# Kernel tuning notes

Measured on AMD Instinct MI355X. Metric: run time of the kernel, lower is better.

Reference implementation:

```python
import jax, jax.numpy as jnp
import numpy as np

C = 384
NUM_HEADS = 12
WS = 12  # window side
N = WS * WS  # tokens per window = 144
NW = 144  # windows per image
BATCH = 8

def setup_inputs() -> dict:
    key = jax.random.key(0)
    k1, k2, k3, k4, k5, k6, k7 = jax.random.split(key, 7)
    x = jax.random.normal(k1, (BATCH, NW, WS, WS, C), dtype=jnp.float32)
    mask = jax.random.normal(k2, (NW, N, N), dtype=jnp.float32)
    s = 1.0 / np.sqrt(C)
    qkv_w = jax.random.normal(k3, (3 * C, C), dtype=jnp.float32) * s
    qkv_b = jax.random.normal(k4, (3 * C,), dtype=jnp.float32) * 0.02
    proj_w = jax.random.normal(k5, (C, C), dtype=jnp.float32) * s
    proj_b = jax.random.normal(k6, (C,), dtype=jnp.float32) * 0.02
    return {"x": x, "mask": mask, "qkv_w": qkv_w, "qkv_b": qkv_b,
            "proj_w": proj_w, "proj_b": proj_b}

def reference(x, mask, qkv_w, qkv_b, proj_w, proj_b):
    B, nW = x.shape[0], x.shape[1]
    head_dim = C // NUM_HEADS
    scale = head_dim ** -0.5
    # (B_, N, C) windowed tokens
    xw = x.reshape(B * nW, N, C)
    qkv = jnp.einsum('bnc,dc->bnd', xw, qkv_w) + qkv_b  # (B_, N, 3C)
    qkv = qkv.reshape(B * nW, N, 3, NUM_HEADS, head_dim)
    q = qkv[:, :, 0].transpose(0, 2, 1, 3) * scale  # (B_, H, N, hd)
    k = qkv[:, :, 1].transpose(0, 2, 1, 3)
    v = qkv[:, :, 2].transpose(0, 2, 1, 3)
    attn = jnp.einsum('bhnd,bhmd->bhnm', q, k)  # (B_, H, N, N)
    # add window mask: view as (B, nW, H, N, N) + mask[None, :, None]
    attn = attn.reshape(B, nW, NUM_HEADS, N, N) + mask[None, :, None, :, :]
    attn = jax.nn.softmax(attn.reshape(B * nW, NUM_HEADS, N, N), axis=-1)
    out = jnp.einsum('bhnm,bhmd->bhnd', attn, v)  # (B_, H, N, hd)
    out = out.transpose(0, 2, 1, 3).reshape(B * nW, N, C)
    out = jnp.einsum('bnc,dc->bnd', out, proj_w) + proj_b
    return out
```

## Files before the change

### kernel.cpp

```cpp
#include <hip/hip_runtime.h>
#include <stdint.h>

#define TOK 144
#define CD  384
#define NH  12
#define HDIM 32
#define NWIN 1152
#define MASKW 144
#define NQKV 1152

typedef __bf16 bf16_t;
typedef __bf16 bf16x4 __attribute__((ext_vector_type(4)));
typedef __bf16 bf16x8 __attribute__((ext_vector_type(8)));
typedef float  f32x4  __attribute__((ext_vector_type(4)));

__device__ __forceinline__ void gload16(const void* g, void* l) {
    __builtin_amdgcn_global_load_lds(
        (const __attribute__((address_space(1))) uint32_t*)g,
        (__attribute__((address_space(3))) uint32_t*)l, 16, 0, 0);
}

__global__ __launch_bounds__(256) void kpack(const float* __restrict__ qkvw,
                                             const float* __restrict__ projw,
                                             bf16_t* __restrict__ WQf,
                                             bf16_t* __restrict__ WPf)
{
    int t = blockIdx.x * 256 + threadIdx.x;
    const int NQU = 55296;
    const float SCALE = 0.17677669529663687f;
    if (t < NQU) {
        int lane = t & 63;
        int jj = (t >> 6) & 7;
        int kh = (t >> 9) & 1;
        int rest = t >> 10;
        int kk = rest % 6, nb = rest / 6;
        int d = nb * 128 + jj * 16 + (lane & 15);
        int k = kk * 64 + kh * 32 + (lane >> 4) * 8;
        const float* src = qkvw + (size_t)d * 384 + k;
        float4 a = *(const float4*)src;
        float4 b = *(const float4*)(src + 4);
        float s = (d < 384) ? SCALE : 1.0f;
        bf16x8 o = {(bf16_t)(a.x*s), (bf16_t)(a.y*s), (bf16_t)(a.z*s), (bf16_t)(a.w*s),
                    (bf16_t)(b.x*s), (bf16_t)(b.y*s), (bf16_t)(b.z*s), (bf16_t)(b.w*s)};
        *(bf16x8*)(WQf + (size_t)t * 8) = o;
    } else {
        int u = t - NQU;
        int lane = u & 63;
        int jj = (u >> 6) & 7;
        int kh = (u >> 9) & 1;
        int rest = u >> 10;
        int kk = rest % 6, nb = rest / 6;
        int d = nb * 128 + jj * 16 + (lane & 15);
        int k = kk * 64 + kh * 32 + (lane >> 4) * 8;
        const float* src = projw + (size_t)d * 384 + k;
        float4 a = *(const float4*)src;
        float4 b = *(const float4*)(src + 4);
        bf16x8 o = {(bf16_t)a.x, (bf16_t)a.y, (bf16_t)a.z, (bf16_t)a.w,
                    (bf16_t)b.x, (bf16_t)b.y, (bf16_t)b.z, (bf16_t)b.w};
        *(bf16x8*)(WPf + (size_t)u * 8) = o;
    }
}

__global__ __launch_bounds__(256) void kmask(const float* __restrict__ mask,
                                             float* __restrict__ maskR)
{
    int t = blockIdx.x * 256 + threadIdx.x;
    int lane = t & 63;
    int g = t >> 6;
    int nt = g % 9;
    int g2 = g / 9;
    int wv = g2 % 9;
    int wm = g2 / 9;
    const float* src = mask + (size_t)wm * 20736
                     + (wv * 16 + (lane >> 4) * 4) * 144 + nt * 16 + (lane & 15);
    f32x4 v = { src[0], src[144], src[288], src[432] };
    *(f32x4*)(maskR + (size_t)t * 4) = v;
}

__global__ __launch_bounds__(256) void kx(const float* __restrict__ x,
                                          bf16_t* __restrict__ xb, int n8)
{
    int i = blockIdx.x * 256 + threadIdx.x;
    if (i < n8) {
        float4 a = *(const float4*)(x + (size_t)i * 8);
        float4 b = *(const float4*)(x + (size_t)i * 8 + 4);
        bf16x8 o = {(bf16_t)a.x, (bf16_t)a.y, (bf16_t)a.z, (bf16_t)a.w,
                    (bf16_t)b.x, (bf16_t)b.y, (bf16_t)b.z, (bf16_t)b.w};
        *(bf16x8*)(xb + (size_t)i * 8) = o;
    }
}

__global__ __launch_bounds__(256) void k_qkv(const bf16_t* __restrict__ xb,
                                             const bf16_t* __restrict__ WQf,
                                             const float* __restrict__ bias,
                                             bf16_t* __restrict__ Qp,
                                             bf16_t* __restrict__ Kp,
                                             bf16_t* __restrict__ VTp)
{
    int nwg = gridDim.x;
    int orig = blockIdx.x;
    int q8 = nwg >> 3, r8 = nwg & 7;
    int xcd = orig & 7, idx = orig >> 3;
    int wgid = (xcd < r8 ? xcd * (q8 + 1) : r8 * (q8 + 1) + (xcd - r8) * q8) + idx;
    int mb = wgid / 9, nb = wgid % 9;

    __shared__ union SMem {
        bf16_t A[2][128 * 64];
        bf16_t tile[128 * 136];
    } sm;

    int tid = threadIdx.x;
    int lane = tid & 63, wid = tid >> 6;
    int wr = (wid >> 1) * 64, wc = (wid & 1) * 64;
    int l15 = lane & 15, l4 = lane >> 4;
    int lr8 = lane >> 3, lc8 = lane & 7;
    int lc8s = lc8 ^ lr8;

    f32x4 acc[4][4] = {};

    const bf16_t* aG = xb + ((size_t)mb * 128 + wid * 32 + lr8) * 384 + lc8s * 8;

    #pragma unroll
    for (int p = 0; p < 4; ++p)
        gload16(aG + (size_t)p * (8 * 384), &sm.A[0][(wid * 4 + p) * 512]);

    for (int kk = 0; kk < 6; ++kk) {
        int buf = kk & 1;
        __syncthreads();
        if (kk < 5) {
            #pragma unroll
            for (int p = 0; p < 4; ++p)
                gload16(aG + (size_t)p * (8 * 384) + (kk + 1) * 64,
                        &sm.A[buf ^ 1][(wid * 4 + p) * 512]);
        }
        #pragma unroll
        for (int kh = 0; kh < 2; ++kh) {
            bf16x8 af[4], bfr[4];
            #pragma unroll
            for (int j = 0; j < 4; ++j)
                bfr[j] = *(const bf16x8*)(WQf +
                    ((((size_t)(nb * 6 + kk) * 2 + kh) * 8 + (wid & 1) * 4 + j) * 64 + lane) * 8);
            #pragma unroll
            for (int i = 0; i < 4; ++i) {
                int row = wr + i * 16 + l15;
                int slot = (kh * 4 + l4) ^ (l15 & 7);
                af[i] = *(const bf16x8*)&sm.A[buf][row * 64 + slot * 8];
            }
            #pragma unroll
            for (int i = 0; i < 4; ++i)
                #pragma unroll
                for (int j = 0; j < 4; ++j)
                    acc[i][j] = __builtin_amdgcn_mfma_f32_16x16x32_bf16(af[i], bfr[j], acc[i][j], 0, 0, 0);
        }
    }
    __syncthreads();

    const int S = 136;
    const float SCALE = 0.17677669529663687f;
    float scl = (nb < 3) ? SCALE : 1.0f;
    float bv[4];
    #pragma unroll
    for (int j = 0; j < 4; ++j) bv[j] = bias[nb * 128 + wc + j * 16 + l15] * scl;

    #pragma unroll
    for (int i = 0; i < 4; ++i)
        #pragma unroll
        for (int j = 0; j < 4; ++j)
            #pragma unroll
            for (int r = 0; r < 4; ++r)
                sm.tile[(wr + i * 16 + l4 * 4 + r) * S + wc + j * 16 + l15] =
                    (bf16_t)(acc[i][j][r] + bv[j]);
    __syncthreads();

    if (nb < 6) {
        bf16_t* dst = (nb < 3) ? Qp : Kp;
        int db0 = (nb % 3) * 128;
        #pragma unroll
        for (int it = 0; it < 8; ++it) {
            int item = tid + it * 256;
            int row = item >> 4, ch = item & 15;
            bf16x8 v = *(const bf16x8*)&sm.tile[row * S + ch * 8];
            int gr = mb * 128 + row;
            int lw = gr / 144, n = gr - lw * 144;
            int dl = db0 + ch * 8;
            int h = dl >> 5, c32 = dl & 31;
            *(bf16x8*)(dst + (size_t)(lw * 12 + h) * 4608 + n * 32 + c32) = v;
        }
    } else {
        int db0 = (nb - 6) * 128;
        #pragma unroll
        for (int it = 0; it < 8; ++it) {
            int item = tid + it * 256;
            int dl = item & 127;
            int nc = item >> 7;
            int gr0 = mb * 128 + nc * 8;
            int lw = gr0 / 144, n0 = gr0 - lw * 144;
            int rr = db0 + dl;
            int h = rr >> 5, j32 = rr & 31;
            bf16x8 v;
            #pragma unroll
            for (int q = 0; q < 8; ++q)
                v[q] = sm.tile[(nc * 8 + q) * S + dl];
            *(bf16x8*)(VTp + (size_t)(lw * 12 + h) * 4608 + j32 * 144 + n0) = v;
        }
    }
}

__global__ __launch_bounds__(576) void k_attn(const bf16_t* __restrict__ Qp,
                                              const bf16_t* __restrict__ Kp,
                                              const bf16_t* __restrict__ VTp,
                                              const float* __restrict__ maskR,
                                              bf16_t* __restrict__ ao,
                                              int w0)
{
    extern __shared__ char smem[];
    bf16_t* kb  = (bf16_t*)smem;
    bf16_t* vtb = kb + 144 * 40;
    bf16_t* pb  = vtb + 32 * 168;

    int nwg = gridDim.x;
    int orig = blockIdx.x;
    int q8 = nwg >> 3, r8 = nwg & 7;
    int xcd = orig & 7, idx = orig >> 3;
    int wgid = (xcd < r8 ? xcd * (q8 + 1) : r8 * (q8 + 1) + (xcd - r8) * q8) + idx;

    int bw = wgid / 12, h = wgid % 12;
    int W = w0 + bw;
    int wm = W % MASKW;
    size_t base = (size_t)(bw * 12 + h) * 4608;
    int tid = threadIdx.x;

    {
        int row = tid >> 2, c8 = (tid & 3) * 8;
        *(uint4*)&kb[row * 40 + c8] = *(const uint4*)(Kp + base + row * 32 + c8);
        int j = tid / 18, seg = tid % 18;
        *(uint4*)&vtb[j * 168 + seg * 8] = *(const uint4*)(VTp + base + j * 144 + seg * 8);
        if (tid < 64) {
            int jj = tid >> 1, cc = 144 + (tid & 1) * 8;
            uint4 z = {0, 0, 0, 0};
            *(uint4*)&vtb[jj * 168 + cc] = z;
        }
    }
    __syncthreads();

    int lane = tid & 63, wv = tid >> 6;
    int l15 = lane & 15, l4 = lane >> 4;
    int row16 = wv * 16;

    bf16x8 aq = *(const bf16x8*)(Qp + base + (row16 + l15) * 32 + l4 * 8);

    const float* mR = maskR + ((size_t)(wm * 9 + wv) * 9) * 256 + lane * 4;
    f32x4 s[9];
    #pragma unroll
    for (int nt = 0; nt < 9; ++nt) {
        bf16x8 bk = *(const bf16x8*)&kb[(nt * 16 + l15) * 40 + l4 * 8];
        f32x4 mv = *(const f32x4*)(mR + nt * 256);
        s[nt] = __builtin_amdgcn_mfma_f32_16x16x32_bf16(aq, bk, mv, 0, 0, 0);
    }

    float mx[4], sm[4];
    #pragma unroll
    for (int r = 0; r < 4; ++r) {
        float m = s[0][r];
        #pragma unroll
        for (int nt = 1; nt < 9; ++nt) m = fmaxf(m, s[nt][r]);
        #pragma unroll
        for (int off = 1; off < 16; off <<= 1) m = fmaxf(m, __shfl_xor(m, off, 64));
        mx[r] = m;
    }
    #pragma unroll
    for (int r = 0; r < 4; ++r) {
        float sum = 0.f;
        #pragma unroll
        for (int nt = 0; nt < 9; ++nt) {
            float e = __expf(s[nt][r] - mx[r]);
            s[nt][r] = e;
            sum += e;
        }
        #pragma unroll
        for (int off = 1; off < 16; off <<= 1) sum += __shfl_xor(sum, off, 64);
        sm[r] = sum;
    }

    #pragma unroll
    for (int nt = 0; nt < 9; ++nt)
        #pragma unroll
        for (int r = 0; r < 4; ++r)
            pb[(row16 + l4 * 4 + r) * 168 + nt * 16 + l15] = (bf16_t)s[nt][r];
    {
        int rr = lane >> 2, cc = 144 + (lane & 3) * 4;
        uint2 z = {0, 0};
        *(uint2*)&pb[(row16 + rr) * 168 + cc] = z;
    }
    f32x4 o0 = {0.f, 0.f, 0.f, 0.f}, o1 = {0.f, 0.f, 0.f, 0.f};
    #pragma unroll
    for (int ks = 0; ks < 5; ++ks) {
        bf16x8 ap  = *(const bf16x8*)&pb[(row16 + l15) * 168 + ks * 32 + l4 * 8];
        bf16x8 bv0 = *(const bf16x8*)&vtb[(l15) * 168 + ks * 32 + l4 * 8];
        bf16x8 bv1 = *(const bf16x8*)&vtb[(16 + l15) * 168 + ks * 32 + l4 * 8];
        o0 = __builtin_amdgcn_mfma_f32_16x16x32_bf16(ap, bv0, o0, 0, 0, 0);
        o1 = __builtin_amdgcn_mfma_f32_16x16x32_bf16(ap, bv1, o1, 0, 0, 0);
    }
    float inv[4];
    #pragma unroll
    for (int r = 0; r < 4; ++r) inv[r] = 1.0f / sm[r];
    bf16_t* ob = pb + row16 * 168;
    #pragma unroll
    for (int r = 0; r < 4; ++r) {
        ob[(l4 * 4 + r) * 32 + l15]      = (bf16_t)(o0[r] * inv[r]);
        ob[(l4 * 4 + r) * 32 + 16 + l15] = (bf16_t)(o1[r] * inv[r]);
    }
    bf16x8 v = *(const bf16x8*)&ob[(lane >> 2) * 32 + (lane & 3) * 8];
    *(bf16x8*)(ao + ((size_t)bw * 144 + row16 + (lane >> 2)) * 384 + h * 32 + (lane & 3) * 8) = v;
}

__global__ __launch_bounds__(256) void k_proj(const bf16_t* __restrict__ ao,
                                              const bf16_t* __restrict__ WPf,
                                              const float* __restrict__ bias,
                                              float* __restrict__ out,
                                              int rowoff)
{
    int nwg = gridDim.x;
    int orig = blockIdx.x;
    int q8 = nwg >> 3, r8 = nwg & 7;
    int xcd = orig & 7, idx = orig >> 3;
    int wgid = (xcd < r8 ? xcd * (q8 + 1) : r8 * (q8 + 1) + (xcd - r8) * q8) + idx;
    int mb = wgid / 3, nb = wgid % 3;

    __shared__ union SMem {
        bf16_t A[2][128 * 64];
        float tile[128 * 68];
    } sm;

    int tid = threadIdx.x;
    int lane = tid & 63, wid = tid >> 6;
    int wr = (wid >> 1) * 64, wc = (wid & 1) * 64;
    int l15 = lane & 15, l4 = lane >> 4;
    int lr8 = lane >> 3, lc8 = lane & 7;
    int lc8s = lc8 ^ lr8;

    f32x4 acc[4][4] = {};

    const bf16_t* aG = ao + ((size_t)mb * 128 + wid * 32 + lr8) * 384 + lc8s * 8;

    #pragma unroll
    for (int p = 0; p < 4; ++p)
        gload16(aG + (size_t)p * (8 * 384), &sm.A[0][(wid * 4 + p) * 512]);

    for (int kk = 0; kk < 6; ++kk) {
        int buf = kk & 1;
        __syncthreads();
        if (kk < 5) {
            #pragma unroll
            for (int p = 0; p < 4; ++p)
                gload16(aG + (size_t)p * (8 * 384) + (kk + 1) * 64,
                        &sm.A[buf ^ 1][(wid * 4 + p) * 512]);
        }
        #pragma unroll
        for (int kh = 0; kh < 2; ++kh) {
            bf16x8 af[4], bfr[4];
            #pragma unroll
            for (int j = 0; j < 4; ++j)
                bfr[j] = *(const bf16x8*)(WPf +
                    ((((size_t)(nb * 6 + kk) * 2 + kh) * 8 + (wid & 1) * 4 + j) * 64 + lane) * 8);
            #pragma unroll
            for (int i = 0; i < 4; ++i) {
                int row = wr + i * 16 + l15;
                int slot = (kh * 4 + l4) ^ (l15 & 7);
                af[i] = *(const bf16x8*)&sm.A[buf][row * 64 + slot * 8];
            }
            #pragma unroll
            for (int i = 0; i < 4; ++i)
                #pragma unroll
                for (int j = 0; j < 4; ++j)
                    acc[i][j] = __builtin_amdgcn_mfma_f32_16x16x32_bf16(af[i], bfr[j], acc[i][j], 0, 0, 0);
        }
    }
    __syncthreads();

    float bv[4];
    #pragma unroll
    for (int j = 0; j < 4; ++j) bv[j] = bias[nb * 128 + wc + j * 16 + l15];

    #pragma unroll
    for (int half = 0; half < 2; ++half) {
        if (half) __syncthreads();
        if ((wid & 1) == half) {
            #pragma unroll
            for (int i = 0; i < 4; ++i)
                #pragma unroll
                for (int j = 0; j < 4; ++j)
                    #pragma unroll
                    for (int r = 0; r < 4; ++r)
                        sm.tile[(wr + i * 16 + l4 * 4 + r) * 68 + j * 16 + l15] =
                            acc[i][j][r] + bv[j];
        }
        __syncthreads();
        #pragma unroll
        for (int it = 0; it < 8; ++it) {
            int item = tid + it * 256;
            int row = item >> 4, ch = item & 15;
            float4 v = *(const float4*)&sm.tile[row * 68 + ch * 4];
            *(float4*)(out + (size_t)(rowoff + mb * 128 + row) * 384
                           + nb * 128 + half * 64 + ch * 4) = v;
        }
    }
}

extern "C" void kernel_launch(void* const* d_in, const int* in_sizes, int n_in,
                              void* d_out, int out_size, void* d_ws, size_t ws_size,
                              hipStream_t stream)
{
    const float* x     = (const float*)d_in[0];
    const float* mask  = (const float*)d_in[1];
    const float* qkvw  = (const float*)d_in[2];
    const float* qkvb  = (const float*)d_in[3];
    const float* projw = (const float*)d_in[4];
    const float* projb = (const float*)d_in[5];
    float* out = (float*)d_out;

    char* ws = (char*)d_ws;
    bf16_t* WQf  = (bf16_t*)ws;
    bf16_t* WPf  = (bf16_t*)(ws + 884736);
    float* maskR = (float*)(ws + 1179648);
    char* chunkbase = ws + 13123584;

    size_t avail = ws_size > 13123584 ? ws_size - 13123584 : 0;
    long cw = (long)(avail / 552960);
    cw = (cw / 16) * 16;
    if (cw > NWIN) cw = NWIN;
    if (cw < 16) cw = 16;

    size_t qbytes = (size_t)cw * 110592;
    bf16_t* Xb  = (bf16_t*)chunkbase;
    bf16_t* Qp  = (bf16_t*)(chunkbase + qbytes);
    bf16_t* Kp  = (bf16_t*)(chunkbase + 2 * qbytes);
    bf16_t* VTp = (bf16_t*)(chunkbase + 3 * qbytes);
    bf16_t* AO  = (bf16_t*)(chunkbase + 4 * qbytes);

    kpack<<<288, 256, 0, stream>>>(qkvw, projw, WQf, WPf);
    kmask<<<2916, 256, 0, stream>>>(mask, maskR);

    for (int w0 = 0; w0 < NWIN; w0 += (int)cw) {
        int c = (int)((NWIN - w0) < cw ? (NWIN - w0) : cw);
        int n8 = c * 6912;
        kx<<<(n8 + 255) / 256, 256, 0, stream>>>(x + (size_t)w0 * 144 * 384, Xb, n8);
        int mblocks = (c * 144) / 128;
        k_qkv<<<mblocks * 9, 256, 0, stream>>>(Xb, WQf, qkvb, Qp, Kp, VTp);
        k_attn<<<c * 12, 576, 70656, stream>>>(Qp, Kp, VTp, maskR, AO, w0);
        k_proj<<<mblocks * 3, 256, 0, stream>>>(AO, WPf, projb, out, w0 * 144);
    }
}
```

Baseline: 647.6 us.

## Load GEMM A fragments directly from global instead of LDS double buffering

Both the QKV and projection GEMM kernels drop their async global-to-LDS double-buffered staging of the A tile. Each wave now reads its MFMA A fragments straight from global memory, relying on L1/L2 for reuse across the two waves that share rows. This removes the per-k-step barriers and the LDS traffic, and shrinks shared memory to just the epilogue tile, which may raise occupancy. The cost is redundant global loads and exposed load latency without explicit prefetch.

```diff
diff --git a/kernel.cpp b/kernel.cpp
--- a/kernel.cpp
+++ b/kernel.cpp
@@ -13,12 +13,6 @@
 typedef __bf16 bf16x4 __attribute__((ext_vector_type(4)));
 typedef __bf16 bf16x8 __attribute__((ext_vector_type(8)));
 typedef float  f32x4  __attribute__((ext_vector_type(4)));
-
-__device__ __forceinline__ void gload16(const void* g, void* l) {
-    __builtin_amdgcn_global_load_lds(
-        (const __attribute__((address_space(1))) uint32_t*)g,
-        (__attribute__((address_space(3))) uint32_t*)l, 16, 0, 0);
-}
 
 __global__ __launch_bounds__(256) void kpack(const float* __restrict__ qkvw,
                                              const float* __restrict__ projw,
@@ -104,48 +98,28 @@
     int wgid = (xcd < r8 ? xcd * (q8 + 1) : r8 * (q8 + 1) + (xcd - r8) * q8) + idx;
     int mb = wgid / 9, nb = wgid % 9;
 
-    __shared__ union SMem {
-        bf16_t A[2][128 * 64];
-        bf16_t tile[128 * 136];
-    } sm;
+    __shared__ bf16_t tile[128 * 136];
 
     int tid = threadIdx.x;
     int lane = tid & 63, wid = tid >> 6;
     int wr = (wid >> 1) * 64, wc = (wid & 1) * 64;
     int l15 = lane & 15, l4 = lane >> 4;
-    int lr8 = lane >> 3, lc8 = lane & 7;
-    int lc8s = lc8 ^ lr8;
 
     f32x4 acc[4][4] = {};
 
-    const bf16_t* aG = xb + ((size_t)mb * 128 + wid * 32 + lr8) * 384 + lc8s * 8;
-
-    #pragma unroll
-    for (int p = 0; p < 4; ++p)
-        gload16(aG + (size_t)p * (8 * 384), &sm.A[0][(wid * 4 + p) * 512]);
+    const bf16_t* aRow = xb + ((size_t)mb * 128 + wr + l15) * 384 + l4 * 8;
+    const bf16_t* bBase = WQf + ((size_t)nb * 96 + (wid & 1) * 4) * 512 + lane * 8;
 
     for (int kk = 0; kk < 6; ++kk) {
-        int buf = kk & 1;
-        __syncthreads();
-        if (kk < 5) {
-            #pragma unroll
-            for (int p = 0; p < 4; ++p)
-                gload16(aG + (size_t)p * (8 * 384) + (kk + 1) * 64,
-                        &sm.A[buf ^ 1][(wid * 4 + p) * 512]);
-        }
         #pragma unroll
         for (int kh = 0; kh < 2; ++kh) {
             bf16x8 af[4], bfr[4];
             #pragma unroll
             for (int j = 0; j < 4; ++j)
-                bfr[j] = *(const bf16x8*)(WQf +
-                    ((((size_t)(nb * 6 + kk) * 2 + kh) * 8 + (wid & 1) * 4 + j) * 64 + lane) * 8);
-            #pragma unroll
-            for (int i = 0; i < 4; ++i) {
-                int row = wr + i * 16 + l15;
-                int slot = (kh * 4 + l4) ^ (l15 & 7);
-                af[i] = *(const bf16x8*)&sm.A[buf][row * 64 + slot * 8];
-            }
+                bfr[j] = *(const bf16x8*)(bBase + ((size_t)(kk * 2 + kh) * 8 + j) * 512);
+            #pragma unroll
+            for (int i = 0; i < 4; ++i)
+                af[i] = *(const bf16x8*)(aRow + (size_t)i * (16 * 384) + kk * 64 + kh * 32);
             #pragma unroll
             for (int i = 0; i < 4; ++i)
                 #pragma unroll
@@ -153,7 +127,6 @@
                     acc[i][j] = __builtin_amdgcn_mfma_f32_16x16x32_bf16(af[i], bfr[j], acc[i][j], 0, 0, 0);
         }
     }
-    __syncthreads();
 
     const int S = 136;
     const float SCALE = 0.17677669529663687f;
@@ -168,7 +141,7 @@
         for (int j = 0; j < 4; ++j)
             #pragma unroll
             for (int r = 0; r < 4; ++r)
-                sm.tile[(wr + i * 16 + l4 * 4 + r) * S + wc + j * 16 + l15] =
+                tile[(wr + i * 16 + l4 * 4 + r) * S + wc + j * 16 + l15] =
                     (bf16_t)(acc[i][j][r] + bv[j]);
     __syncthreads();
 
@@ -179,7 +152,7 @@
         for (int it = 0; it < 8; ++it) {
             int item = tid + it * 256;
             int row = item >> 4, ch = item & 15;
-            bf16x8 v = *(const bf16x8*)&sm.tile[row * S + ch * 8];
+            bf16x8 v = *(const bf16x8*)&tile[row * S + ch * 8];
             int gr = mb * 128 + row;
             int lw = gr / 144, n = gr - lw * 144;
             int dl = db0 + ch * 8;
@@ -200,7 +173,7 @@
             bf16x8 v;
             #pragma unroll
             for (int q = 0; q < 8; ++q)
-                v[q] = sm.tile[(nc * 8 + q) * S + dl];
+                v[q] = tile[(nc * 8 + q) * S + dl];
             *(bf16x8*)(VTp + (size_t)(lw * 12 + h) * 4608 + j32 * 144 + n0) = v;
         }
     }
@@ -327,48 +300,28 @@
     int wgid = (xcd < r8 ? xcd * (q8 + 1) : r8 * (q8 + 1) + (xcd - r8) * q8) + idx;
     int mb = wgid / 3, nb = wgid % 3;
 
-    __shared__ union SMem {
-        bf16_t A[2][128 * 64];
-        float tile[128 * 68];
-    } sm;
+    __shared__ float tile[128 * 68];
 
     int tid = threadIdx.x;
     int lane = tid & 63, wid = tid >> 6;
     int wr = (wid >> 1) * 64, wc = (wid & 1) * 64;
     int l15 = lane & 15, l4 = lane >> 4;
-    int lr8 = lane >> 3, lc8 = lane & 7;
-    int lc8s = lc8 ^ lr8;
 
     f32x4 acc[4][4] = {};
 
-    const bf16_t* aG = ao + ((size_t)mb * 128 + wid * 32 + lr8) * 384 + lc8s * 8;
-
-    #pragma unroll
-    for (int p = 0; p < 4; ++p)
-        gload16(aG + (size_t)p * (8 * 384), &sm.A[0][(wid * 4 + p) * 512]);
+    const bf16_t* aRow = ao + ((size_t)mb * 128 + wr + l15) * 384 + l4 * 8;
+    const bf16_t* bBase = WPf + ((size_t)nb * 96 + (wid & 1) * 4) * 512 + lane * 8;
 
     for (int kk = 0; kk < 6; ++kk) {
-        int buf = kk & 1;
-        __syncthreads();
-        if (kk < 5) {
-            #pragma unroll
-            for (int p = 0; p < 4; ++p)
-                gload16(aG + (size_t)p * (8 * 384) + (kk + 1) * 64,
-                        &sm.A[buf ^ 1][(wid * 4 + p) * 512]);
-        }
         #pragma unroll
         for (int kh = 0; kh < 2; ++kh) {
             bf16x8 af[4], bfr[4];
             #pragma unroll
             for (int j = 0; j < 4; ++j)
-                bfr[j] = *(const bf16x8*)(WPf +
-                    ((((size_t)(nb * 6 + kk) * 2 + kh) * 8 + (wid & 1) * 4 + j) * 64 + lane) * 8);
-            #pragma unroll
-            for (int i = 0; i < 4; ++i) {
-                int row = wr + i * 16 + l15;
-                int slot = (kh * 4 + l4) ^ (l15 & 7);
-                af[i] = *(const bf16x8*)&sm.A[buf][row * 64 + slot * 8];
-            }
+                bfr[j] = *(const bf16x8*)(bBase + ((size_t)(kk * 2 + kh) * 8 + j) * 512);
+            #pragma unroll
+            for (int i = 0; i < 4; ++i)
+                af[i] = *(const bf16x8*)(aRow + (size_t)i * (16 * 384) + kk * 64 + kh * 32);
             #pragma unroll
             for (int i = 0; i < 4; ++i)
                 #pragma unroll
@@ -376,7 +329,6 @@
                     acc[i][j] = __builtin_amdgcn_mfma_f32_16x16x32_bf16(af[i], bfr[j], acc[i][j], 0, 0, 0);
         }
     }
-    __syncthreads();
 
     float bv[4];
     #pragma unroll
@@ -392,7 +344,7 @@
                 for (int j = 0; j < 4; ++j)
                     #pragma unroll
                     for (int r = 0; r < 4; ++r)
-                        sm.tile[(wr + i * 16 + l4 * 4 + r) * 68 + j * 16 + l15] =
+                        tile[(wr + i * 16 + l4 * 4 + r) * 68 + j * 16 + l15] =
                             acc[i][j][r] + bv[j];
         }
         __syncthreads();
@@ -400,7 +352,7 @@
         for (int it = 0; it < 8; ++it) {
             int item = tid + it * 256;
             int row = item >> 4, ch = item & 15;
-            float4 v = *(const float4*)&sm.tile[row * 68 + ch * 4];
+            float4 v = *(const float4*)&tile[row * 68 + ch * 4];
             *(float4*)(out + (size_t)(rowoff + mb * 128 + row) * 384
                            + nb * 128 + half * 64 + ch * 4) = v;
         }
```

New measurement: 820.2 us. 26.7% more time.

## Make QKV kernel keep whole A row-tile in LDS and loop over all output blocks

Applied to the files above, without the earlier changes.

The QKV GEMM now launches one workgroup per 128-row M tile instead of one per (M, N) tile pair. Each workgroup loads the full 128x384 bf16 A tile into dynamic LDS once, then iterates over all nine 128-column output blocks. Each output block goes through a per-wave staging tile, so the epilogue needs no block-wide barriers. This removes the repeated A loads and the double-buffer synchronisation, and drops the XCD block remapping. In exchange the grid shrinks ninefold and each block needs about 132 KB of LDS, which cuts occupancy and leaves no overlap between the A load and the MFMA work.

```diff
diff --git a/kernel.cpp b/kernel.cpp
--- a/kernel.cpp
+++ b/kernel.cpp
@@ -97,111 +97,100 @@
                                              bf16_t* __restrict__ Kp,
                                              bf16_t* __restrict__ VTp)
 {
-    int nwg = gridDim.x;
-    int orig = blockIdx.x;
-    int q8 = nwg >> 3, r8 = nwg & 7;
-    int xcd = orig & 7, idx = orig >> 3;
-    int wgid = (xcd < r8 ? xcd * (q8 + 1) : r8 * (q8 + 1) + (xcd - r8) * q8) + idx;
-    int mb = wgid / 9, nb = wgid % 9;
-
-    __shared__ union SMem {
-        bf16_t A[2][128 * 64];
-        bf16_t tile[128 * 136];
-    } sm;
+    extern __shared__ char smem[];
+    bf16_t* A = (bf16_t*)smem;
 
     int tid = threadIdx.x;
     int lane = tid & 63, wid = tid >> 6;
+    bf16_t* pt = (bf16_t*)(smem + 98304) + wid * 4608;
+
+    int mb = blockIdx.x;
     int wr = (wid >> 1) * 64, wc = (wid & 1) * 64;
     int l15 = lane & 15, l4 = lane >> 4;
     int lr8 = lane >> 3, lc8 = lane & 7;
     int lc8s = lc8 ^ lr8;
 
-    f32x4 acc[4][4] = {};
-
-    const bf16_t* aG = xb + ((size_t)mb * 128 + wid * 32 + lr8) * 384 + lc8s * 8;
-
-    #pragma unroll
-    for (int p = 0; p < 4; ++p)
-        gload16(aG + (size_t)p * (8 * 384), &sm.A[0][(wid * 4 + p) * 512]);
-
-    for (int kk = 0; kk < 6; ++kk) {
-        int buf = kk & 1;
-        __syncthreads();
-        if (kk < 5) {
-            #pragma unroll
-            for (int p = 0; p < 4; ++p)
-                gload16(aG + (size_t)p * (8 * 384) + (kk + 1) * 64,
-                        &sm.A[buf ^ 1][(wid * 4 + p) * 512]);
-        }
-        #pragma unroll
-        for (int kh = 0; kh < 2; ++kh) {
-            bf16x8 af[4], bfr[4];
+    const size_t rowbase = (size_t)mb * 128;
+
+    #pragma unroll
+    for (int p = 0; p < 24; ++p) {
+        int unit = wid * 24 + p;
+        int kk = unit >> 4, rg = unit & 15;
+        const bf16_t* src = xb + (rowbase + rg * 8 + lr8) * 384 + kk * 64 + lc8s * 8;
+        gload16(src, A + (size_t)unit * 512);
+    }
+    __syncthreads();
+
+    const float SCALE = 0.17677669529663687f;
+
+    #pragma unroll 1
+    for (int nb = 0; nb < 9; ++nb) {
+        f32x4 acc[4][4] = {};
+        const bf16_t* bBase = WQf + ((size_t)nb * 96 + (wid & 1) * 4) * 512 + lane * 8;
+
+        #pragma unroll
+        for (int kk = 0; kk < 6; ++kk) {
+            #pragma unroll
+            for (int kh = 0; kh < 2; ++kh) {
+                bf16x8 af[4], bfr[4];
+                #pragma unroll
+                for (int j = 0; j < 4; ++j)
+                    bfr[j] = *(const bf16x8*)(bBase + ((size_t)(kk * 2 + kh) * 8 + j) * 512);
+                #pragma unroll
+                for (int i = 0; i < 4; ++i) {
+                    int row = wr + i * 16 + l15;
+                    int slot = (kh * 4 + l4) ^ (l15 & 7);
+                    af[i] = *(const bf16x8*)&A[((size_t)kk * 128 + row) * 64 + slot * 8];
+                }
+                #pragma unroll
+                for (int i = 0; i < 4; ++i)
+                    #pragma unroll
+                    for (int j = 0; j < 4; ++j)
+                        acc[i][j] = __builtin_amdgcn_mfma_f32_16x16x32_bf16(af[i], bfr[j], acc[i][j], 0, 0, 0);
+            }
+        }
+
+        float scl = (nb < 3) ? SCALE : 1.0f;
+        float bv[4];
+        #pragma unroll
+        for (int j = 0; j < 4; ++j) bv[j] = bias[nb * 128 + wc + j * 16 + l15] * scl;
+
+        #pragma unroll
+        for (int i = 0; i < 4; ++i)
             #pragma unroll
             for (int j = 0; j < 4; ++j)
-                bfr[j] = *(const bf16x8*)(WQf +
-                    ((((size_t)(nb * 6 + kk) * 2 + kh) * 8 + (wid & 1) * 4 + j) * 64 + lane) * 8);
-            #pragma unroll
-            for (int i = 0; i < 4; ++i) {
-                int row = wr + i * 16 + l15;
-                int slot = (kh * 4 + l4) ^ (l15 & 7);
-                af[i] = *(const bf16x8*)&sm.A[buf][row * 64 + slot * 8];
+                #pragma unroll
+                for (int r = 0; r < 4; ++r)
+                    pt[(i * 16 + l4 * 4 + r) * 72 + j * 16 + l15] =
+                        (bf16_t)(acc[i][j][r] + bv[j]);
+
+        if (nb < 6) {
+            bf16_t* dst = (nb < 3) ? Qp : Kp;
+            int db0 = (nb % 3) * 128 + wc;
+            #pragma unroll
+            for (int rr = 0; rr < 8; ++rr) {
+                int lrow = rr * 8 + lr8;
+                bf16x8 v = *(const bf16x8*)&pt[lrow * 72 + lc8 * 8];
+                int gr = (int)rowbase + wr + lrow;
+                int lw = gr / 144, n = gr - lw * 144;
+                int d = db0 + lc8 * 8;
+                int h = d >> 5, c32 = d & 31;
+                *(bf16x8*)(dst + (size_t)(lw * 12 + h) * 4608 + n * 32 + c32) = v;
             }
-            #pragma unroll
-            for (int i = 0; i < 4; ++i)
-                #pragma unroll
-                for (int j = 0; j < 4; ++j)
-                    acc[i][j] = __builtin_amdgcn_mfma_f32_16x16x32_bf16(af[i], bfr[j], acc[i][j], 0, 0, 0);
-        }
-    }
-    __syncthreads();
-
-    const int S = 136;
-    const float SCALE = 0.17677669529663687f;
-    float scl = (nb < 3) ? SCALE : 1.0f;
-    float bv[4];
-    #pragma unroll
-    for (int j = 0; j < 4; ++j) bv[j] = bias[nb * 128 + wc + j * 16 + l15] * scl;
-
-    #pragma unroll
-    for (int i = 0; i < 4; ++i)
-        #pragma unroll
-        for (int j = 0; j < 4; ++j)
-            #pragma unroll
-            for (int r = 0; r < 4; ++r)
-                sm.tile[(wr + i * 16 + l4 * 4 + r) * S + wc + j * 16 + l15] =
-                    (bf16_t)(acc[i][j][r] + bv[j]);
-    __syncthreads();
-
-    if (nb < 6) {
-        bf16_t* dst = (nb < 3) ? Qp : Kp;
-        int db0 = (nb % 3) * 128;
-        #pragma unroll
-        for (int it = 0; it < 8; ++it) {
-            int item = tid + it * 256;
-            int row = item >> 4, ch = item & 15;
-            bf16x8 v = *(const bf16x8*)&sm.tile[row * S + ch * 8];
-            int gr = mb * 128 + row;
-            int lw = gr / 144, n = gr - lw * 144;
-            int dl = db0 + ch * 8;
-            int h = dl >> 5, c32 = dl & 31;
-            *(bf16x8*)(dst + (size_t)(lw * 12 + h) * 4608 + n * 32 + c32) = v;
-        }
-    } else {
-        int db0 = (nb - 6) * 128;
-        #pragma unroll
-        for (int it = 0; it < 8; ++it) {
-            int item = tid + it * 256;
-            int dl = item & 127;
-            int nc = item >> 7;
-            int gr0 = mb * 128 + nc * 8;
-            int lw = gr0 / 144, n0 = gr0 - lw * 144;
-            int rr = db0 + dl;
-            int h = rr >> 5, j32 = rr & 31;
-            bf16x8 v;
-            #pragma unroll
-            for (int q = 0; q < 8; ++q)
-                v[q] = sm.tile[(nc * 8 + q) * S + dl];
-            *(bf16x8*)(VTp + (size_t)(lw * 12 + h) * 4608 + j32 * 144 + n0) = v;
+        } else {
+            int db0 = (nb - 6) * 128 + wc;
+            #pragma unroll
+            for (int nc = 0; nc < 8; ++nc) {
+                int gr0 = (int)rowbase + wr + nc * 8;
+                int lw = gr0 / 144, n0 = gr0 - lw * 144;
+                int rr2 = db0 + lane;
+                int h = rr2 >> 5, j32 = rr2 & 31;
+                bf16x8 v;
+                #pragma unroll
+                for (int q = 0; q < 8; ++q)
+                    v[q] = pt[(nc * 8 + q) * 72 + lane];
+                *(bf16x8*)(VTp + (size_t)(lw * 12 + h) * 4608 + j32 * 144 + n0) = v;
+            }
         }
     }
 }
@@ -446,7 +435,7 @@
         int n8 = c * 6912;
         kx<<<(n8 + 255) / 256, 256, 0, stream>>>(x + (size_t)w0 * 144 * 384, Xb, n8);
         int mblocks = (c * 144) / 128;
-        k_qkv<<<mblocks * 9, 256, 0, stream>>>(Xb, WQf, qkvb, Qp, Kp, VTp);
+        k_qkv<<<mblocks, 256, 135168, stream>>>(Xb, WQf, qkvb, Qp, Kp, VTp);
         k_attn<<<c * 12, 576, 70656, stream>>>(Qp, Kp, VTp, maskR, AO, w0);
         k_proj<<<mblocks * 3, 256, 0, stream>>>(AO, WPf, projb, out, w0 * 144);
     }
```

New measurement: 818.7 us. 26.4% more time.

## Fuse fp32-to-bf16 input conversion into QKV GEMM and add MFMA priority hints

Applied to the files above, without the earlier changes.

Removes the separate kx conversion kernel and the Xb buffer. k_qkv now reads fp32 x directly, converts it to bf16 in registers and stores it into swizzled LDS, replacing the async global_load_lds path. It also wraps the attention MFMA loops in s_setprio to raise wave priority, and shrinks per-window workspace so chunks can be larger. The trade-off is that k_qkv now reads twice the bytes per element and loses asynchronous LDS loads, though a full write and re-read of bf16 x is saved.

```diff
diff --git a/kernel.cpp b/kernel.cpp
--- a/kernel.cpp
+++ b/kernel.cpp
@@ -77,20 +77,7 @@
     *(f32x4*)(maskR + (size_t)t * 4) = v;
 }
 
-__global__ __launch_bounds__(256) void kx(const float* __restrict__ x,
-                                          bf16_t* __restrict__ xb, int n8)
-{
-    int i = blockIdx.x * 256 + threadIdx.x;
-    if (i < n8) {
-        float4 a = *(const float4*)(x + (size_t)i * 8);
-        float4 b = *(const float4*)(x + (size_t)i * 8 + 4);
-        bf16x8 o = {(bf16_t)a.x, (bf16_t)a.y, (bf16_t)a.z, (bf16_t)a.w,
-                    (bf16_t)b.x, (bf16_t)b.y, (bf16_t)b.z, (bf16_t)b.w};
-        *(bf16x8*)(xb + (size_t)i * 8) = o;
-    }
-}
-
-__global__ __launch_bounds__(256) void k_qkv(const bf16_t* __restrict__ xb,
+__global__ __launch_bounds__(256) void k_qkv(const float* __restrict__ x,
                                              const bf16_t* __restrict__ WQf,
                                              const float* __restrict__ bias,
                                              bf16_t* __restrict__ Qp,
@@ -114,32 +101,48 @@
     int wr = (wid >> 1) * 64, wc = (wid & 1) * 64;
     int l15 = lane & 15, l4 = lane >> 4;
     int lr8 = lane >> 3, lc8 = lane & 7;
-    int lc8s = lc8 ^ lr8;
+
+    int sr = tid >> 3;
+    int sc = tid & 7;
+    int scs = sc ^ (sr & 7);
 
     f32x4 acc[4][4] = {};
 
-    const bf16_t* aG = xb + ((size_t)mb * 128 + wid * 32 + lr8) * 384 + lc8s * 8;
-
-    #pragma unroll
-    for (int p = 0; p < 4; ++p)
-        gload16(aG + (size_t)p * (8 * 384), &sm.A[0][(wid * 4 + p) * 512]);
+    const size_t rowbase = (size_t)mb * 128;
+    const float* xs = x + (rowbase + sr) * 384 + sc * 8;
+
+    #pragma unroll
+    for (int p = 0; p < 4; ++p) {
+        const float* s4 = xs + (size_t)p * (32 * 384);
+        float4 a = *(const float4*)s4;
+        float4 b = *(const float4*)(s4 + 4);
+        bf16x8 o = {(bf16_t)a.x, (bf16_t)a.y, (bf16_t)a.z, (bf16_t)a.w,
+                    (bf16_t)b.x, (bf16_t)b.y, (bf16_t)b.z, (bf16_t)b.w};
+        *(bf16x8*)&sm.A[0][(sr + 32 * p) * 64 + scs * 8] = o;
+    }
+
+    const bf16_t* bBase = WQf + ((size_t)nb * 96 + (wid & 1) * 4) * 512 + lane * 8;
 
     for (int kk = 0; kk < 6; ++kk) {
         int buf = kk & 1;
         __syncthreads();
         if (kk < 5) {
             #pragma unroll
-            for (int p = 0; p < 4; ++p)
-                gload16(aG + (size_t)p * (8 * 384) + (kk + 1) * 64,
-                        &sm.A[buf ^ 1][(wid * 4 + p) * 512]);
+            for (int p = 0; p < 4; ++p) {
+                const float* s4 = xs + (kk + 1) * 64 + (size_t)p * (32 * 384);
+                float4 a = *(const float4*)s4;
+                float4 b = *(const float4*)(s4 + 4);
+                bf16x8 o = {(bf16_t)a.x, (bf16_t)a.y, (bf16_t)a.z, (bf16_t)a.w,
+                            (bf16_t)b.x, (bf16_t)b.y, (bf16_t)b.z, (bf16_t)b.w};
+                *(bf16x8*)&sm.A[buf ^ 1][(sr + 32 * p) * 64 + scs * 8] = o;
+            }
         }
         #pragma unroll
         for (int kh = 0; kh < 2; ++kh) {
             bf16x8 af[4], bfr[4];
             #pragma unroll
             for (int j = 0; j < 4; ++j)
-                bfr[j] = *(const bf16x8*)(WQf +
-                    ((((size_t)(nb * 6 + kk) * 2 + kh) * 8 + (wid & 1) * 4 + j) * 64 + lane) * 8);
+                bfr[j] = *(const bf16x8*)(bBase + ((size_t)(kk * 16 + kh * 8 + j)) * 512);
             #pragma unroll
             for (int i = 0; i < 4; ++i) {
                 int row = wr + i * 16 + l15;
@@ -251,12 +254,14 @@
 
     const float* mR = maskR + ((size_t)(wm * 9 + wv) * 9) * 256 + lane * 4;
     f32x4 s[9];
+    __builtin_amdgcn_s_setprio(1);
     #pragma unroll
     for (int nt = 0; nt < 9; ++nt) {
         bf16x8 bk = *(const bf16x8*)&kb[(nt * 16 + l15) * 40 + l4 * 8];
         f32x4 mv = *(const f32x4*)(mR + nt * 256);
         s[nt] = __builtin_amdgcn_mfma_f32_16x16x32_bf16(aq, bk, mv, 0, 0, 0);
     }
+    __builtin_amdgcn_s_setprio(0);
 
     float mx[4], sm[4];
     #pragma unroll
@@ -293,6 +298,7 @@
         *(uint2*)&pb[(row16 + rr) * 168 + cc] = z;
     }
     f32x4 o0 = {0.f, 0.f, 0.f, 0.f}, o1 = {0.f, 0.f, 0.f, 0.f};
+    __builtin_amdgcn_s_setprio(1);
     #pragma unroll
     for (int ks = 0; ks < 5; ++ks) {
         bf16x8 ap  = *(const bf16x8*)&pb[(row16 + l15) * 168 + ks * 32 + l4 * 8];
@@ -301,6 +307,7 @@
         o0 = __builtin_amdgcn_mfma_f32_16x16x32_bf16(ap, bv0, o0, 0, 0, 0);
         o1 = __builtin_amdgcn_mfma_f32_16x16x32_bf16(ap, bv1, o1, 0, 0, 0);
     }
+    __builtin_amdgcn_s_setprio(0);
     float inv[4];
     #pragma unroll
     for (int r = 0; r < 4; ++r) inv[r] = 1.0f / sm[r];
@@ -426,27 +433,24 @@
     char* chunkbase = ws + 13123584;
 
     size_t avail = ws_size > 13123584 ? ws_size - 13123584 : 0;
-    long cw = (long)(avail / 552960);
+    long cw = (long)(avail / 442368);
     cw = (cw / 16) * 16;
     if (cw > NWIN) cw = NWIN;
     if (cw < 16) cw = 16;
 
     size_t qbytes = (size_t)cw * 110592;
-    bf16_t* Xb  = (bf16_t*)chunkbase;
-    bf16_t* Qp  = (bf16_t*)(chunkbase + qbytes);
-    bf16_t* Kp  = (bf16_t*)(chunkbase + 2 * qbytes);
-    bf16_t* VTp = (bf16_t*)(chunkbase + 3 * qbytes);
-    bf16_t* AO  = (bf16_t*)(chunkbase + 4 * qbytes);
+    bf16_t* Qp  = (bf16_t*)chunkbase;
+    bf16_t* Kp  = (bf16_t*)(chunkbase + qbytes);
+    bf16_t* VTp = (bf16_t*)(chunkbase + 2 * qbytes);
+    bf16_t* AO  = (bf16_t*)(chunkbase + 3 * qbytes);
 
     kpack<<<288, 256, 0, stream>>>(qkvw, projw, WQf, WPf);
     kmask<<<2916, 256, 0, stream>>>(mask, maskR);
 
     for (int w0 = 0; w0 < NWIN; w0 += (int)cw) {
         int c = (int)((NWIN - w0) < cw ? (NWIN - w0) : cw);
-        int n8 = c * 6912;
-        kx<<<(n8 + 255) / 256, 256, 0, stream>>>(x + (size_t)w0 * 144 * 384, Xb, n8);
         int mblocks = (c * 144) / 128;
-        k_qkv<<<mblocks * 9, 256, 0, stream>>>(Xb, WQf, qkvb, Qp, Kp, VTp);
+        k_qkv<<<mblocks * 9, 256, 0, stream>>>(x + (size_t)w0 * 55296, WQf, qkvb, Qp, Kp, VTp);
         k_attn<<<c * 12, 576, 70656, stream>>>(Qp, Kp, VTp, maskR, AO, w0);
         k_proj<<<mblocks * 3, 256, 0, stream>>>(AO, WPf, projb, out, w0 * 144);
     }
```

New measurement: 727.3 us, median of 6. +12.3%, slower.
